# Kernel optimization log

Measured on AMD Instinct MI355X. Metric: run time of the kernel, lower is better.

Reference implementation:

```python
import jax, jax.numpy as jnp
import numpy as np

B, C, H, W_, N, E = 8, 256, 128, 128, 4096, 128
EPS = 1e-12  # torch F.normalize default eps


def grid_sample_points(x, kpts):
    """Bilinear grid_sample at point coords, padding_mode='zeros', align_corners=False.
    x: [B,C,H,W], kpts: [B,N,2] in [-1,1] (x,y order) -> [B,C,N].
    """
    Bx, Cx, Hx, Wx = x.shape
    # unnormalize (align_corners=False)
    ix = (kpts[..., 0] + 1.0) * (Wx * 0.5) - 0.5  # [B,N]
    iy = (kpts[..., 1] + 1.0) * (Hx * 0.5) - 0.5
    x0f = jnp.floor(ix)
    y0f = jnp.floor(iy)
    wx = ix - x0f  # fractional weights
    wy = iy - y0f
    x0 = x0f.astype(jnp.int32)
    y0 = y0f.astype(jnp.int32)
    x1 = x0 + 1
    y1 = y0 + 1

    def gather(xi, yi):
        valid = (xi >= 0) & (xi < Wx) & (yi >= 0) & (yi < Hx)  # [B,N]
        xc = jnp.clip(xi, 0, Wx - 1)
        yc = jnp.clip(yi, 0, Hx - 1)
        # per-batch gather of [C] vectors at N points -> [B,C,N]
        v = jax.vmap(lambda xb, yy, xx: xb[:, yy, xx])(x, yc, xc)
        return v * valid[:, None, :].astype(x.dtype)

    v00 = gather(x0, y0)
    v10 = gather(x1, y0)
    v01 = gather(x0, y1)
    v11 = gather(x1, y1)
    wxb = wx[:, None, :]
    wyb = wy[:, None, :]
    return (v00 * (1 - wxb) * (1 - wyb)
            + v10 * wxb * (1 - wyb)
            + v01 * (1 - wxb) * wyb
            + v11 * wxb * wyb)


def setup_inputs() -> dict:
    key = jax.random.key(0)
    k1, k2, k3 = jax.random.split(key, 3)
    x = jax.random.normal(k1, (B, C, H, W_), dtype=jnp.float32)
    # keypoints in normalized [-1,1] coords (grid_sample convention)
    kpts = jax.random.uniform(k2, (B, N, 2), dtype=jnp.float32) * 2.0 - 1.0
    # xavier_normal_(gain=0.1) for Linear(C -> E)
    std = 0.1 * np.sqrt(2.0 / (C + E))
    whiten_w = jax.random.normal(k3, (E, C), dtype=jnp.float32) * std
    whiten_b = jnp.zeros((E,), dtype=jnp.float32)
    return {"x": x, "kpts": kpts, "whiten_w": whiten_w, "whiten_b": whiten_b}


def reference(x, kpts, whiten_w, whiten_b):
    desc = grid_sample_points(x, kpts)              # [B,C,N]
    desc = jnp.transpose(desc, (0, 2, 1))           # [B,N,C]
    desc = jnp.einsum('bnc,ec->bne', desc, whiten_w) + whiten_b  # [B,N,E]
    norm = jnp.maximum(jnp.linalg.norm(desc, axis=2, keepdims=True), EPS)
    return desc / norm
```

## Files before the change

kernel.cpp:

```cpp
#include <hip/hip_runtime.h>
#include <hip/hip_bf16.h>
#include <math.h>

#define BB 8
#define CC 256
#define HH 128
#define WW 128
#define NN 4096
#define EE 128

typedef __bf16 bf16x8 __attribute__((ext_vector_type(8)));
typedef float f32x4 __attribute__((ext_vector_type(4)));

#define WF_OFF    0
#define BASE_OFF  65536
#define WGT_OFF   196608
#define DESCF_OFF 720896
#define WS_NEED   (720896ull + 16777216ull)

__global__ __launch_bounds__(256) void prep_kernel(
    const float* __restrict__ kpts, const float* __restrict__ W,
    int* __restrict__ baseb, float4* __restrict__ wgt, __bf16* __restrict__ Wf) {
  int i = blockIdx.x * blockDim.x + threadIdx.x;
  {
    int j = i & 7, lane = (i >> 3) & 63, etile = (i >> 9) & 7, kstep = (i >> 12) & 7;
    int e = etile * 16 + (lane & 15);
    int c = kstep * 32 + ((lane >> 4) << 3) + j;
    Wf[i] = (__bf16)W[e * CC + c];
  }
  float kx = kpts[2 * i], ky = kpts[2 * i + 1];
  float ix = (kx + 1.f) * (WW * 0.5f) - 0.5f;
  float iy = (ky + 1.f) * (HH * 0.5f) - 0.5f;
  float x0f = floorf(ix), y0f = floorf(iy);
  float wx = ix - x0f, wy = iy - y0f;
  int x0 = (int)x0f, y0 = (int)y0f;
  float ax0 = (x0 >= 0 && x0 < WW) ? (1.f - wx) : 0.f;
  float ax1 = (x0 + 1 >= 0 && x0 + 1 < WW) ? wx : 0.f;
  float ay0 = (y0 >= 0 && y0 < HH) ? (1.f - wy) : 0.f;
  float ay1 = (y0 + 1 >= 0 && y0 + 1 < HH) ? wy : 0.f;
  int bx = min(max(x0, 0), WW - 2);
  int by = min(max(y0, 0), HH - 2);
  float a0 = 0.f, a1 = 0.f, c0 = 0.f, c1 = 0.f;
  if (x0 == bx) a0 += ax0; else if (x0 == bx + 1) a1 += ax0;
  if (x0 + 1 == bx) a0 += ax1; else if (x0 + 1 == bx + 1) a1 += ax1;
  if (y0 == by) c0 += ay0; else if (y0 == by + 1) c1 += ay0;
  if (y0 + 1 == by) c0 += ay1; else if (y0 + 1 == by + 1) c1 += ay1;
  baseb[i] = by * WW + bx;
  wgt[i] = make_float4(a0 * c0, a1 * c0, a0 * c1, a1 * c1);
}

__global__ __launch_bounds__(512) void gather_kernel(
    const float* __restrict__ x, const int* __restrict__ baseb,
    const float4* __restrict__ wgt, __bf16* __restrict__ descf) {
  __shared__ float plane[HH * WW];
  int blk = blockIdx.x;
  int b = blk >> 8, c = blk & 255;
  int t = threadIdx.x;
  const float4* s4 = (const float4*)(x + ((size_t)blk << 14));
  float4* p4 = (float4*)plane;
#pragma unroll
  for (int i = 0; i < 8; ++i) p4[t + 512 * i] = s4[t + 512 * i];
  __syncthreads();
  const int* bb = baseb + b * NN;
  const float4* wb = wgt + b * NN;
  __bf16* dst = descf + ((b << 20) + ((c >> 5) << 9) + (((c >> 3) & 3) << 7) + (c & 7));
#pragma unroll
  for (int i = 0; i < 8; ++i) {
    int n = t + 512 * i;
    int base = bb[n];
    float4 w = wb[n];
    float v = plane[base] * w.x + plane[base + 1] * w.y
            + plane[base + WW] * w.z + plane[base + WW + 1] * w.w;
    dst[((n >> 4) << 12) + ((n & 15) << 3)] = (__bf16)v;
  }
}

__global__ __launch_bounds__(256) void gemm_norm_kernel(
    const __bf16* __restrict__ descf, const __bf16* __restrict__ Wf,
    const float* __restrict__ bias, float* __restrict__ out) {
  __shared__ __bf16 wlds[8 * 8 * 64 * 8];
  int t = threadIdx.x;
  {
    const float4* src = (const float4*)Wf;
    float4* d = (float4*)wlds;
#pragma unroll
    for (int i = 0; i < 16; ++i) d[t + 256 * i] = src[t + 256 * i];
  }
  __syncthreads();
  int blk = blockIdx.x;
  int b = blk >> 6;
  int wave = t >> 6, lane = t & 63;
  int ntile = ((blk & 63) << 2) + wave;
  const bf16x8* bsrc =
      (const bf16x8*)(descf + ((size_t)b << 20) + ((size_t)ntile << 12));
  bf16x8 bfrag[8];
#pragma unroll
  for (int k = 0; k < 8; ++k) bfrag[k] = bsrc[k * 64 + lane];
  const bf16x8* alds = (const bf16x8*)wlds;
  f32x4 acc[8];
#pragma unroll
  for (int e = 0; e < 8; ++e) acc[e] = (f32x4)(0.f);
#pragma unroll
  for (int k = 0; k < 8; ++k) {
#pragma unroll
    for (int e = 0; e < 8; ++e) {
      bf16x8 a = alds[(k * 8 + e) * 64 + lane];
      acc[e] = __builtin_amdgcn_mfma_f32_16x16x32_bf16(a, bfrag[k], acc[e], 0, 0, 0);
    }
  }
  int quad = lane >> 4, col = lane & 15;
  int n = ntile * 16 + col;
  float s = 0.f;
  float4 av[8];
#pragma unroll
  for (int e = 0; e < 8; ++e) {
    float4 bi = *(const float4*)(bias + e * 16 + quad * 4);
    float4 v = make_float4(acc[e][0] + bi.x, acc[e][1] + bi.y,
                           acc[e][2] + bi.z, acc[e][3] + bi.w);
    av[e] = v;
    s += v.x * v.x + v.y * v.y + v.z * v.z + v.w * v.w;
  }
  s += __shfl_xor(s, 16);
  s += __shfl_xor(s, 32);
  float inv = 1.f / fmaxf(sqrtf(s), 1e-12f);
  float4* out4 = (float4*)out + (((size_t)(b * NN + n)) << 5) + quad;
#pragma unroll
  for (int e = 0; e < 8; ++e)
    out4[e * 4] = make_float4(av[e].x * inv, av[e].y * inv,
                              av[e].z * inv, av[e].w * inv);
}

__global__ __launch_bounds__(128) void fused_fallback(
    const float* __restrict__ x, const float* __restrict__ kpts,
    const float* __restrict__ W, const float* __restrict__ bias,
    float* __restrict__ out) {
  __shared__ float dsc[CC];
  __shared__ float sred[2];
  int blk = blockIdx.x;
  int b = blk >> 12;
  float kx = kpts[2 * blk], ky = kpts[2 * blk + 1];
  float ix = (kx + 1.f) * (WW * 0.5f) - 0.5f;
  float iy = (ky + 1.f) * (HH * 0.5f) - 0.5f;
  float x0f = floorf(ix), y0f = floorf(iy);
  float wx = ix - x0f, wy = iy - y0f;
  int x0 = (int)x0f, y0 = (int)y0f;
  float ax0 = (x0 >= 0 && x0 < WW) ? (1.f - wx) : 0.f;
  float ax1 = (x0 + 1 >= 0 && x0 + 1 < WW) ? wx : 0.f;
  float ay0 = (y0 >= 0 && y0 < HH) ? (1.f - wy) : 0.f;
  float ay1 = (y0 + 1 >= 0 && y0 + 1 < HH) ? wy : 0.f;
  int bx = min(max(x0, 0), WW - 2);
  int by = min(max(y0, 0), HH - 2);
  float a0 = 0.f, a1 = 0.f, r0 = 0.f, r1 = 0.f;
  if (x0 == bx) a0 += ax0; else if (x0 == bx + 1) a1 += ax0;
  if (x0 + 1 == bx) a0 += ax1; else if (x0 + 1 == bx + 1) a1 += ax1;
  if (y0 == by) r0 += ay0; else if (y0 == by + 1) r1 += ay0;
  if (y0 + 1 == by) r0 += ay1; else if (y0 + 1 == by + 1) r1 += ay1;
  int base = by * WW + bx;
  float w00 = a0 * r0, w10 = a1 * r0, w01 = a0 * r1, w11 = a1 * r1;
  int t = threadIdx.x;
  const float* src = x + ((size_t)b << 22);
  for (int c = t; c < CC; c += 128) {
    const float* p = src + ((size_t)c << 14);
    dsc[c] = p[base] * w00 + p[base + 1] * w10 + p[base + WW] * w01 + p[base + WW + 1] * w11;
  }
  __syncthreads();
  float acc = bias[t];
  const float* wr = W + t * CC;
  for (int c = 0; c < CC; ++c) acc += wr[c] * dsc[c];
  float s = acc * acc;
  for (int m = 1; m < 64; m <<= 1) s += __shfl_xor(s, m);
  if ((t & 63) == 0) sred[t >> 6] = s;
  __syncthreads();
  float tot = sred[0] + sred[1];
  float inv = 1.f / fmaxf(sqrtf(tot), 1e-12f);
  out[((size_t)blk << 7) + t] = acc * inv;
}

extern "C" void kernel_launch(void* const* d_in, const int* in_sizes, int n_in,
                              void* d_out, int out_size, void* d_ws, size_t ws_size,
                              hipStream_t stream) {
  const float* x    = (const float*)d_in[0];
  const float* kpts = (const float*)d_in[1];
  const float* W    = (const float*)d_in[2];
  const float* bias = (const float*)d_in[3];
  float* out = (float*)d_out;
  if (ws_size >= WS_NEED) {
    char* ws = (char*)d_ws;
    __bf16* Wf    = (__bf16*)(ws + WF_OFF);
    int* baseb    = (int*)(ws + BASE_OFF);
    float4* wgt   = (float4*)(ws + WGT_OFF);
    __bf16* descf = (__bf16*)(ws + DESCF_OFF);
    prep_kernel<<<BB * NN / 256, 256, 0, stream>>>(kpts, W, baseb, wgt, Wf);
    gather_kernel<<<BB * CC, 512, 0, stream>>>(x, baseb, wgt, descf);
    gemm_norm_kernel<<<BB * (NN / 64), 256, 0, stream>>>(descf, Wf, bias, out);
  } else {
    fused_fallback<<<BB * NN, 128, 0, stream>>>(x, kpts, W, bias, out);
  }
}
```

Before: 222.1 us.

## Fuse keypoint prep into gather, batch 8 channels per block with double-buffered planes

Removes the separate prep kernel by computing bilinear bases and weights inside the gather kernel, and converts the W matrix there too. Each block now processes 8 channels of one batch, reusing the per-point coordinates across channels and prefetching the next channel plane into registers while sampling the current one from double-buffered LDS. Results are packed into 16-byte bf16x8 stores instead of scattered 2-byte writes. The grid shrinks to 256 blocks each using 128 KB of LDS, which lowers occupancy and parallelism.

```diff
diff --git a/kernel.cpp b/kernel.cpp
--- a/kernel.cpp
+++ b/kernel.cpp
@@ -13,65 +13,91 @@
 typedef float f32x4 __attribute__((ext_vector_type(4)));
 
 #define WF_OFF    0
-#define BASE_OFF  65536
-#define WGT_OFF   196608
-#define DESCF_OFF 720896
-#define WS_NEED   (720896ull + 16777216ull)
-
-__global__ __launch_bounds__(256) void prep_kernel(
-    const float* __restrict__ kpts, const float* __restrict__ W,
-    int* __restrict__ baseb, float4* __restrict__ wgt, __bf16* __restrict__ Wf) {
-  int i = blockIdx.x * blockDim.x + threadIdx.x;
-  {
+#define DESCF_OFF 65536
+#define WS_NEED   (65536ull + 16777216ull)
+
+__global__ __launch_bounds__(512, 2) void gather_kernel(
+    const float* __restrict__ x, const float* __restrict__ kpts,
+    const float* __restrict__ W, __bf16* __restrict__ descf,
+    __bf16* __restrict__ Wf) {
+  __shared__ float buf[2][HH * WW];
+  int blk = blockIdx.x;
+  int b = blk >> 5, g = blk & 31;
+  int t = threadIdx.x;
+  const float4* x4 = (const float4*)(x + ((size_t)((b << 8) + (g << 3)) << 14));
+  float4 r0[8], r1[8];
+#pragma unroll
+  for (int q = 0; q < 8; ++q) r0[q] = x4[t + 512 * q];
+#pragma unroll
+  for (int q = 0; q < 8; ++q) r1[q] = x4[4096 + t + 512 * q];
+  if (t < 128) {
+    int i = (blk << 7) + t;
     int j = i & 7, lane = (i >> 3) & 63, etile = (i >> 9) & 7, kstep = (i >> 12) & 7;
-    int e = etile * 16 + (lane & 15);
-    int c = kstep * 32 + ((lane >> 4) << 3) + j;
-    Wf[i] = (__bf16)W[e * CC + c];
-  }
-  float kx = kpts[2 * i], ky = kpts[2 * i + 1];
-  float ix = (kx + 1.f) * (WW * 0.5f) - 0.5f;
-  float iy = (ky + 1.f) * (HH * 0.5f) - 0.5f;
-  float x0f = floorf(ix), y0f = floorf(iy);
-  float wx = ix - x0f, wy = iy - y0f;
-  int x0 = (int)x0f, y0 = (int)y0f;
-  float ax0 = (x0 >= 0 && x0 < WW) ? (1.f - wx) : 0.f;
-  float ax1 = (x0 + 1 >= 0 && x0 + 1 < WW) ? wx : 0.f;
-  float ay0 = (y0 >= 0 && y0 < HH) ? (1.f - wy) : 0.f;
-  float ay1 = (y0 + 1 >= 0 && y0 + 1 < HH) ? wy : 0.f;
-  int bx = min(max(x0, 0), WW - 2);
-  int by = min(max(y0, 0), HH - 2);
-  float a0 = 0.f, a1 = 0.f, c0 = 0.f, c1 = 0.f;
-  if (x0 == bx) a0 += ax0; else if (x0 == bx + 1) a1 += ax0;
-  if (x0 + 1 == bx) a0 += ax1; else if (x0 + 1 == bx + 1) a1 += ax1;
-  if (y0 == by) c0 += ay0; else if (y0 == by + 1) c1 += ay0;
-  if (y0 + 1 == by) c0 += ay1; else if (y0 + 1 == by + 1) c1 += ay1;
-  baseb[i] = by * WW + bx;
-  wgt[i] = make_float4(a0 * c0, a1 * c0, a0 * c1, a1 * c1);
-}
-
-__global__ __launch_bounds__(512) void gather_kernel(
-    const float* __restrict__ x, const int* __restrict__ baseb,
-    const float4* __restrict__ wgt, __bf16* __restrict__ descf) {
-  __shared__ float plane[HH * WW];
-  int blk = blockIdx.x;
-  int b = blk >> 8, c = blk & 255;
-  int t = threadIdx.x;
-  const float4* s4 = (const float4*)(x + ((size_t)blk << 14));
-  float4* p4 = (float4*)plane;
-#pragma unroll
-  for (int i = 0; i < 8; ++i) p4[t + 512 * i] = s4[t + 512 * i];
-  __syncthreads();
-  const int* bb = baseb + b * NN;
-  const float4* wb = wgt + b * NN;
-  __bf16* dst = descf + ((b << 20) + ((c >> 5) << 9) + (((c >> 3) & 3) << 7) + (c & 7));
+    Wf[i] = (__bf16)W[(etile * 16 + (lane & 15)) * CC + kstep * 32 + ((lane >> 4) << 3) + j];
+  }
+  int base[8];
+  float4 wt[8];
+  const float2* kp = (const float2*)(kpts + ((size_t)(b * NN) << 1));
 #pragma unroll
   for (int i = 0; i < 8; ++i) {
-    int n = t + 512 * i;
-    int base = bb[n];
-    float4 w = wb[n];
-    float v = plane[base] * w.x + plane[base + 1] * w.y
-            + plane[base + WW] * w.z + plane[base + WW + 1] * w.w;
-    dst[((n >> 4) << 12) + ((n & 15) << 3)] = (__bf16)v;
+    int n = t + (i << 9);
+    float2 k2 = kp[n];
+    float ix = (k2.x + 1.f) * (WW * 0.5f) - 0.5f;
+    float iy = (k2.y + 1.f) * (HH * 0.5f) - 0.5f;
+    float x0f = floorf(ix), y0f = floorf(iy);
+    float wx = ix - x0f, wy = iy - y0f;
+    int x0 = (int)x0f, y0 = (int)y0f;
+    float ax0 = (x0 >= 0 && x0 < WW) ? (1.f - wx) : 0.f;
+    float ax1 = (x0 + 1 >= 0 && x0 + 1 < WW) ? wx : 0.f;
+    float ay0 = (y0 >= 0 && y0 < HH) ? (1.f - wy) : 0.f;
+    float ay1 = (y0 + 1 >= 0 && y0 + 1 < HH) ? wy : 0.f;
+    int bx = min(max(x0, 0), WW - 2);
+    int by = min(max(y0, 0), HH - 2);
+    float a0 = 0.f, a1 = 0.f, c0 = 0.f, c1 = 0.f;
+    if (x0 == bx) a0 += ax0; else if (x0 == bx + 1) a1 += ax0;
+    if (x0 + 1 == bx) a0 += ax1; else if (x0 + 1 == bx + 1) a1 += ax1;
+    if (y0 == by) c0 += ay0; else if (y0 == by + 1) c1 += ay0;
+    if (y0 + 1 == by) c0 += ay1; else if (y0 + 1 == by + 1) c1 += ay1;
+    base[i] = by * WW + bx;
+    wt[i] = make_float4(a0 * c0, a1 * c0, a0 * c1, a1 * c1);
+  }
+  bf16x8 res[8];
+#pragma unroll
+  for (int p = 0; p < 8; ++p) {
+    float* bcur = buf[p & 1];
+    float4* b4 = (float4*)bcur;
+    if (p & 1) {
+#pragma unroll
+      for (int q = 0; q < 8; ++q) b4[t + 512 * q] = r1[q];
+    } else {
+#pragma unroll
+      for (int q = 0; q < 8; ++q) b4[t + 512 * q] = r0[q];
+    }
+    __syncthreads();
+    if (p + 2 < 8) {
+      if (p & 1) {
+#pragma unroll
+        for (int q = 0; q < 8; ++q) r1[q] = x4[(p + 2) * 4096 + t + 512 * q];
+      } else {
+#pragma unroll
+        for (int q = 0; q < 8; ++q) r0[q] = x4[(p + 2) * 4096 + t + 512 * q];
+      }
+    }
+#pragma unroll
+    for (int i = 0; i < 8; ++i) {
+      int bs = base[i];
+      float4 w = wt[i];
+      float v = bcur[bs] * w.x + bcur[bs + 1] * w.y
+              + bcur[bs + WW] * w.z + bcur[bs + WW + 1] * w.w;
+      res[i][p] = (__bf16)v;
+    }
+  }
+#pragma unroll
+  for (int i = 0; i < 8; ++i) {
+    int n = t + (i << 9);
+    size_t a16 = ((size_t)b << 17) + ((size_t)(n >> 4) << 9)
+               + ((size_t)(g >> 2) << 6) + ((size_t)(g & 3) << 4) + (n & 15);
+    *(bf16x8*)(descf + (a16 << 3)) = res[i];
   }
 }
 
@@ -187,11 +213,8 @@
   if (ws_size >= WS_NEED) {
     char* ws = (char*)d_ws;
     __bf16* Wf    = (__bf16*)(ws + WF_OFF);
-    int* baseb    = (int*)(ws + BASE_OFF);
-    float4* wgt   = (float4*)(ws + WGT_OFF);
     __bf16* descf = (__bf16*)(ws + DESCF_OFF);
-    prep_kernel<<<BB * NN / 256, 256, 0, stream>>>(kpts, W, baseb, wgt, Wf);
-    gather_kernel<<<BB * CC, 512, 0, stream>>>(x, baseb, wgt, descf);
+    gather_kernel<<<BB * 32, 512, 0, stream>>>(x, kpts, W, descf, Wf);
     gemm_norm_kernel<<<BB * (NN / 64), 256, 0, stream>>>(descf, Wf, bias, out);
   } else {
     fused_fallback<<<BB * NN, 128, 0, stream>>>(x, kpts, W, bias, out);
```

Measured after the change: 259.7 us. 1.17x slower.
